# Optimization experiments

Measured on AMD Instinct MI355X. Metric: run time of the kernel, lower is better.

## Reference

```python
import jax, jax.numpy as jnp
import numpy as np

N_HEAD = 16
N_EMBD = 1024
TIME_EMBD = 64
EPS = 1e-5

def _ln(x, w, b):
    mu = jnp.mean(x, axis=-1, keepdims=True)
    var = jnp.mean(jnp.square(x - mu), axis=-1, keepdims=True)
    return (x - mu) * jax.lax.rsqrt(var + EPS) * w + b

def _gelu(x):
    return jax.nn.gelu(x, approximate=False)

def setup_inputs() -> dict:
    key = jax.random.key(0)
    ks = jax.random.split(key, 12)
    B, T, D, TE = 2, 2048, N_EMBD, TIME_EMBD
    C = D + TE  # 1088
    s = lambda fan_in: 1.0 / np.sqrt(fan_in)
    return {
        "z": jax.random.normal(ks[0], (B, T, D), jnp.float32),
        "t": jax.random.uniform(ks[1], (B,), jnp.float32),
        # time_mlp: Linear(1, TE) -> GELU -> Linear(TE, TE)
        "w_t1": jax.random.normal(ks[2], (1, TE), jnp.float32) * s(1),
        "b_t1": jnp.zeros((TE,), jnp.float32),
        "w_t2": jax.random.normal(ks[3], (TE, TE), jnp.float32) * s(TE),
        "b_t2": jnp.zeros((TE,), jnp.float32),
        # attention
        "ln_a_w": jnp.ones((C,), jnp.float32),
        "ln_a_b": jnp.zeros((C,), jnp.float32),
        "w_attn": jax.random.normal(ks[4], (C, 3 * D), jnp.float32) * s(C),
        "b_attn": jnp.zeros((3 * D,), jnp.float32),
        "w_proj": jax.random.normal(ks[5], (D, D), jnp.float32) * s(D),
        "b_proj": jnp.zeros((D,), jnp.float32),
        # mlp
        "ln_m_w": jnp.ones((C,), jnp.float32),
        "ln_m_b": jnp.zeros((C,), jnp.float32),
        "w_fc": jax.random.normal(ks[6], (C, 4 * D), jnp.float32) * s(C),
        "b_fc": jnp.zeros((4 * D,), jnp.float32),
        "w_fc2": jax.random.normal(ks[7], (4 * D, D), jnp.float32) * s(4 * D),
        "b_fc2": jnp.zeros((D,), jnp.float32),
    }

def reference(z, t, w_t1, b_t1, w_t2, b_t2, ln_a_w, ln_a_b, w_attn, b_attn,
              w_proj, b_proj, ln_m_w, ln_m_b, w_fc, b_fc, w_fc2, b_fc2):
    B, T, D = z.shape
    H, hd = N_HEAD, N_EMBD // N_HEAD
    # time embedding: [B, TE] broadcast over T
    t_emb = _gelu(t[:, None] @ w_t1 + b_t1) @ w_t2 + b_t2
    t_emb_bt = jnp.broadcast_to(t_emb[:, None, :], (B, T, TIME_EMBD))
    # --- attention with time-conditioned input ---
    zt = jnp.concatenate([z, t_emb_bt], axis=-1)            # [B,T,D+TE]
    x = _ln(zt, ln_a_w, ln_a_b)
    qkv = x @ w_attn + b_attn                               # [B,T,3D]
    q, k, v = jnp.split(qkv, 3, axis=-1)
    q = q.reshape(B, T, H, hd)
    k = k.reshape(B, T, H, hd)
    v = v.reshape(B, T, H, hd)
    att = jnp.einsum('bqhd,bkhd->bhqk', q, k) * (1.0 / np.sqrt(hd))
    mask = jnp.tril(jnp.ones((T, T), bool))
    att = jnp.where(mask, att, -jnp.inf)
    att = jax.nn.softmax(att, axis=-1)
    y = jnp.einsum('bhqk,bkhd->bqhd', att, v).reshape(B, T, D)
    h = y @ w_proj + b_proj                                 # [B,T,D]
    # --- mlp with time-conditioned input ---
    ht = jnp.concatenate([h, t_emb_bt], axis=-1)
    m = _ln(ht, ln_m_w, ln_m_b)
    dz = _gelu(m @ w_fc + b_fc) @ w_fc2 + b_fc2             # [B,T,D]
    return dz
```

## Files before the change

kernel.cpp:

```cpp
#include <hip/hip_runtime.h>
#include <stdint.h>
#include <math.h>

#define T_SEQ 2048
#define NHEAD 16
#define HD 64
#define DMODEL 1024
#define CDIM 1088
#define MROWS 4096

typedef uint16_t u16;
typedef __bf16 b8v __attribute__((ext_vector_type(8)));
typedef float f4v __attribute__((ext_vector_type(4)));

typedef __attribute__((address_space(3))) void lds_void;
typedef const __attribute__((address_space(1))) void glb_void;

__device__ __forceinline__ float b2f(u16 u) {
  union { uint32_t i; float f; } c; c.i = ((uint32_t)u) << 16; return c.f;
}
__device__ __forceinline__ u16 f2b(float f) {
  union { float f; uint32_t i; } c; c.f = f;
  uint32_t x = c.i;
  return (u16)((x + 0x7fffu + ((x >> 16) & 1u)) >> 16);
}
__device__ __forceinline__ float gelu_f(float x) {
  return 0.5f * x * (1.0f + erff(x * 0.70710678118654752f));
}

__global__ void time_mlp_kernel(const float* __restrict__ t, const float* __restrict__ w1,
                                const float* __restrict__ b1, const float* __restrict__ w2,
                                const float* __restrict__ b2, float* __restrict__ temb) {
  __shared__ float h1[2][64];
  int tid = threadIdx.x;
  int b = tid >> 6, i = tid & 63;
  float tv = t[b];
  h1[b][i] = gelu_f(tv * w1[i] + b1[i]);
  __syncthreads();
  float acc = b2[i];
  for (int k = 0; k < 64; ++k) acc += h1[b][k] * w2[k * 64 + i];
  temb[b * 64 + i] = acc;
}

__global__ __launch_bounds__(256) void transpose_kernel(const float* __restrict__ src,
                                                        u16* __restrict__ dst,
                                                        int R, int C) {
  __shared__ u16 tile[32][33];
  int tx = threadIdx.x & 31, ty = threadIdx.x >> 5;
  int c0 = blockIdx.x * 32, r0 = blockIdx.y * 32;
#pragma unroll
  for (int i = 0; i < 4; ++i) {
    int r = ty + i * 8;
    tile[r][tx] = f2b(src[(size_t)(r0 + r) * C + c0 + tx]);
  }
  __syncthreads();
#pragma unroll
  for (int i = 0; i < 4; ++i) {
    int c = ty + i * 8;
    dst[(size_t)(c0 + c) * R + r0 + tx] = tile[tx][c];
  }
}

__global__ __launch_bounds__(256) void ln_concat_kernel(const float* __restrict__ zf,
                                                        const u16* __restrict__ zb,
                                                        const float* __restrict__ temb,
                                                        const float* __restrict__ w,
                                                        const float* __restrict__ bvec,
                                                        u16* __restrict__ xout,
                                                        int in_f32) {
  __shared__ float red[4];
  int row = blockIdx.x;
  int b = row / T_SEQ;
  int tid = threadIdx.x;
  float v[5];
  float sum = 0.f;
#pragma unroll
  for (int i = 0; i < 5; ++i) {
    int c = tid + i * 256;
    float val = 0.f;
    if (c < CDIM) {
      if (c < DMODEL)
        val = in_f32 ? zf[(size_t)row * DMODEL + c] : b2f(zb[(size_t)row * DMODEL + c]);
      else
        val = temb[b * 64 + (c - DMODEL)];
    }
    v[i] = val;
    sum += val;
  }
#pragma unroll
  for (int off = 32; off; off >>= 1) sum += __shfl_xor(sum, off, 64);
  int wv = tid >> 6, ln = tid & 63;
  if (ln == 0) red[wv] = sum;
  __syncthreads();
  float mean = (red[0] + red[1] + red[2] + red[3]) * (1.0f / CDIM);
  __syncthreads();
  float sq = 0.f;
#pragma unroll
  for (int i = 0; i < 5; ++i) {
    int c = tid + i * 256;
    if (c < CDIM) { float d = v[i] - mean; sq += d * d; }
  }
#pragma unroll
  for (int off = 32; off; off >>= 1) sq += __shfl_xor(sq, off, 64);
  if (ln == 0) red[wv] = sq;
  __syncthreads();
  float inv = rsqrtf((red[0] + red[1] + red[2] + red[3]) * (1.0f / CDIM) + 1e-5f);
#pragma unroll
  for (int i = 0; i < 5; ++i) {
    int c = tid + i * 256;
    if (c < CDIM)
      xout[(size_t)row * CDIM + c] = f2b((v[i] - mean) * inv * w[c] + bvec[c]);
  }
}

__global__ __launch_bounds__(256) void gemm_bt_kernel(const u16* __restrict__ A,
                                                      const u16* __restrict__ Bt,
                                                      const float* __restrict__ bias,
                                                      void* __restrict__ Cout,
                                                      int M, int N, int K,
                                                      int do_gelu, int out_f32) {
  __shared__ u16 As[2][128 * 32];
  __shared__ u16 Bs[2][128 * 32];
  const int tid = threadIdx.x;
  const int wave = tid >> 6, lane = tid & 63;
  const int wr = wave >> 1, wc = wave & 1;
  const int m0 = blockIdx.x * 128;
  const int n0 = blockIdx.y * 128;
  const int lrow = lane & 15, quad = lane >> 4;
  const int srow = lane >> 2, sseg = lane & 3;

  const u16* gA0 = A  + (size_t)(m0 + wave * 32 + srow) * K + sseg * 8;
  const u16* gA1 = gA0 + (size_t)16 * K;
  const u16* gB0 = Bt + (size_t)(n0 + wave * 32 + srow) * K + sseg * 8;
  const u16* gB1 = gB0 + (size_t)16 * K;
  const int la0 = (wave * 32) * 32, la1 = (wave * 32 + 16) * 32;

  f4v acc[4][4] = {};

  __builtin_amdgcn_global_load_lds((glb_void*)gA0, (lds_void*)&As[0][la0], 16, 0, 0);
  __builtin_amdgcn_global_load_lds((glb_void*)gA1, (lds_void*)&As[0][la1], 16, 0, 0);
  __builtin_amdgcn_global_load_lds((glb_void*)gB0, (lds_void*)&Bs[0][la0], 16, 0, 0);
  __builtin_amdgcn_global_load_lds((glb_void*)gB1, (lds_void*)&Bs[0][la1], 16, 0, 0);

  int cur = 0;
  for (int k0 = 0; k0 < K; k0 += 32) {
    __syncthreads();
    if (k0 + 32 < K) {
      int nxt = cur ^ 1;
      __builtin_amdgcn_global_load_lds((glb_void*)(gA0 + k0 + 32), (lds_void*)&As[nxt][la0], 16, 0, 0);
      __builtin_amdgcn_global_load_lds((glb_void*)(gA1 + k0 + 32), (lds_void*)&As[nxt][la1], 16, 0, 0);
      __builtin_amdgcn_global_load_lds((glb_void*)(gB0 + k0 + 32), (lds_void*)&Bs[nxt][la0], 16, 0, 0);
      __builtin_amdgcn_global_load_lds((glb_void*)(gB1 + k0 + 32), (lds_void*)&Bs[nxt][la1], 16, 0, 0);
    }
    b8v af[4], bfr[4];
#pragma unroll
    for (int mi = 0; mi < 4; ++mi)
      af[mi] = *(const b8v*)(&As[cur][(wr * 64 + mi * 16 + lrow) * 32 + quad * 8]);
#pragma unroll
    for (int ni = 0; ni < 4; ++ni)
      bfr[ni] = *(const b8v*)(&Bs[cur][(wc * 64 + ni * 16 + lrow) * 32 + quad * 8]);
#pragma unroll
    for (int mi = 0; mi < 4; ++mi)
#pragma unroll
      for (int ni = 0; ni < 4; ++ni)
        acc[mi][ni] = __builtin_amdgcn_mfma_f32_16x16x32_bf16(af[mi], bfr[ni], acc[mi][ni], 0, 0, 0);
    cur ^= 1;
  }

#pragma unroll
  for (int mi = 0; mi < 4; ++mi) {
#pragma unroll
    for (int ni = 0; ni < 4; ++ni) {
      int gcol = n0 + wc * 64 + ni * 16 + lrow;
      float bv = bias[gcol];
#pragma unroll
      for (int r = 0; r < 4; ++r) {
        int grow = m0 + wr * 64 + mi * 16 + quad * 4 + r;
        float v = acc[mi][ni][r] + bv;
        if (do_gelu) v = gelu_f(v);
        if (out_f32)
          ((float*)Cout)[(size_t)grow * N + gcol] = v;
        else
          ((u16*)Cout)[(size_t)grow * N + gcol] = f2b(v);
      }
    }
  }
}

__global__ __launch_bounds__(256) void attn_mfma_kernel(const u16* __restrict__ qkv,
                                                        u16* __restrict__ y) {
  __shared__ u16 Ks[64 * 72];
  __shared__ u16 Vts[64 * 72];
  __shared__ u16 Ps[128 * 72];
  const int bh = blockIdx.x;
  const int b = bh >> 4, h = bh & 15;
  const int yb = blockIdx.y;
  const int qt = (yb < 8) ? (yb * 2) : (31 - yb * 2);
  const int tid = threadIdx.x, w = tid >> 6, lane = tid & 63;
  const int lrow = lane & 15, quad = lane >> 4;
  const int q0 = qt * 128;

  b8v qf[2][2];
#pragma unroll
  for (int s = 0; s < 2; ++s)
#pragma unroll
    for (int dc = 0; dc < 2; ++dc) {
      int row = q0 + w * 32 + s * 16 + lrow;
      qf[s][dc] = *(const b8v*)(qkv + (size_t)(b * T_SEQ + row) * 3072 + h * 64 + dc * 32 + quad * 8);
    }

  f4v oacc[2][4] = {};
  float mst[2][4], lst[2][4];
#pragma unroll
  for (int s = 0; s < 2; ++s)
#pragma unroll
    for (int r = 0; r < 4; ++r) { mst[s][r] = -__builtin_inff(); lst[s][r] = 0.f; }

  const int nch = 2 * qt + 2;
  for (int ct = 0; ct < nch; ++ct) {
    __syncthreads();
    {
      int r = tid >> 2, sg = tid & 3;
      const u16* src = qkv + (size_t)(b * T_SEQ + ct * 64 + r) * 3072 + h * 64 + 1024 + sg * 16;
      uint4 k1 = *(const uint4*)(src);
      uint4 k2 = *(const uint4*)(src + 8);
      *(uint4*)(&Ks[r * 72 + sg * 16]) = k1;
      *(uint4*)(&Ks[r * 72 + sg * 16 + 8]) = k2;
    }
    {
      int pr = tid >> 3, dsg = tid & 7;
      const u16* v0 = qkv + (size_t)(b * T_SEQ + ct * 64 + 2 * pr) * 3072 + h * 64 + 2048 + dsg * 8;
      uint4 a = *(const uint4*)(v0);
      uint4 bb = *(const uint4*)(v0 + 3072);
      uint32_t aw[4] = {a.x, a.y, a.z, a.w};
      uint32_t bw[4] = {bb.x, bb.y, bb.z, bb.w};
#pragma unroll
      for (int j = 0; j < 8; ++j) {
        int d = dsg * 8 + j;
        u16 ae = (u16)(aw[j >> 1] >> ((j & 1) * 16));
        u16 be = (u16)(bw[j >> 1] >> ((j & 1) * 16));
        int keyp = (2 * pr) ^ (((d >> 3) & 7) * 8);
        *(uint32_t*)(&Vts[d * 72 + keyp]) = (uint32_t)ae | ((uint32_t)be << 16);
      }
    }
    __syncthreads();

    f4v sacc[2][4] = {};
    b8v kf[4][2];
#pragma unroll
    for (int ks = 0; ks < 4; ++ks)
#pragma unroll
      for (int dc = 0; dc < 2; ++dc)
        kf[ks][dc] = *(const b8v*)(&Ks[(ks * 16 + lrow) * 72 + dc * 32 + quad * 8]);
#pragma unroll
    for (int s = 0; s < 2; ++s)
#pragma unroll
      for (int ks = 0; ks < 4; ++ks)
#pragma unroll
        for (int dc = 0; dc < 2; ++dc)
          sacc[s][ks] = __builtin_amdgcn_mfma_f32_16x16x32_bf16(qf[s][dc], kf[ks][dc], sacc[s][ks], 0, 0, 0);

    bool diag = (ct >= 2 * qt);
#pragma unroll
    for (int s = 0; s < 2; ++s)
#pragma unroll
      for (int ks = 0; ks < 4; ++ks) {
        int col = ct * 64 + ks * 16 + lrow;
#pragma unroll
        for (int r = 0; r < 4; ++r) {
          float v = sacc[s][ks][r] * 0.125f;
          int row = q0 + w * 32 + s * 16 + quad * 4 + r;
          if (diag && col > row) v = -__builtin_inff();
          sacc[s][ks][r] = v;
        }
      }

#pragma unroll
    for (int s = 0; s < 2; ++s) {
#pragma unroll
      for (int r = 0; r < 4; ++r) {
        float rmax = fmaxf(fmaxf(sacc[s][0][r], sacc[s][1][r]), fmaxf(sacc[s][2][r], sacc[s][3][r]));
#pragma unroll
        for (int off = 1; off < 16; off <<= 1) rmax = fmaxf(rmax, __shfl_xor(rmax, off, 64));
        float mn = fmaxf(mst[s][r], rmax);
        float al = __expf(mst[s][r] - mn);
        mst[s][r] = mn;
        float psum = 0.f;
#pragma unroll
        for (int ks = 0; ks < 4; ++ks) {
          float p = __expf(sacc[s][ks][r] - mn);
          sacc[s][ks][r] = p;
          psum += p;
        }
#pragma unroll
        for (int off = 1; off < 16; off <<= 1) psum += __shfl_xor(psum, off, 64);
        lst[s][r] = lst[s][r] * al + psum;
#pragma unroll
        for (int ds = 0; ds < 4; ++ds) oacc[s][ds][r] *= al;
      }
    }

#pragma unroll
    for (int s = 0; s < 2; ++s)
#pragma unroll
      for (int ks = 0; ks < 4; ++ks)
#pragma unroll
        for (int r = 0; r < 4; ++r)
          Ps[(w * 32 + s * 16 + quad * 4 + r) * 72 + ks * 16 + lrow] = f2b(sacc[s][ks][r]);

    b8v pf[2][2], vf[4][2];
#pragma unroll
    for (int s = 0; s < 2; ++s)
#pragma unroll
      for (int kc = 0; kc < 2; ++kc)
        pf[s][kc] = *(const b8v*)(&Ps[(w * 32 + s * 16 + lrow) * 72 + kc * 32 + quad * 8]);
#pragma unroll
    for (int ds = 0; ds < 4; ++ds)
#pragma unroll
      for (int kc = 0; kc < 2; ++kc) {
        int d = ds * 16 + lrow;
        int off = (kc * 32 + quad * 8) ^ (((d >> 3) & 7) * 8);
        vf[ds][kc] = *(const b8v*)(&Vts[d * 72 + off]);
      }
#pragma unroll
    for (int s = 0; s < 2; ++s)
#pragma unroll
      for (int ds = 0; ds < 4; ++ds)
#pragma unroll
        for (int kc = 0; kc < 2; ++kc)
          oacc[s][ds] = __builtin_amdgcn_mfma_f32_16x16x32_bf16(pf[s][kc], vf[ds][kc], oacc[s][ds], 0, 0, 0);
  }

#pragma unroll
  for (int s = 0; s < 2; ++s)
#pragma unroll
    for (int ds = 0; ds < 4; ++ds)
#pragma unroll
      for (int r = 0; r < 4; ++r) {
        int row = q0 + w * 32 + s * 16 + quad * 4 + r;
        y[(size_t)(b * T_SEQ + row) * DMODEL + h * 64 + ds * 16 + lrow] =
            f2b(oacc[s][ds][r] / lst[s][r]);
      }
}

extern "C" void kernel_launch(void* const* d_in, const int* in_sizes, int n_in,
                              void* d_out, int out_size, void* d_ws, size_t ws_size,
                              hipStream_t stream) {
  const float* z      = (const float*)d_in[0];
  const float* t      = (const float*)d_in[1];
  const float* w_t1   = (const float*)d_in[2];
  const float* b_t1   = (const float*)d_in[3];
  const float* w_t2   = (const float*)d_in[4];
  const float* b_t2   = (const float*)d_in[5];
  const float* ln_a_w = (const float*)d_in[6];
  const float* ln_a_b = (const float*)d_in[7];
  const float* w_attn = (const float*)d_in[8];
  const float* b_attn = (const float*)d_in[9];
  const float* w_proj = (const float*)d_in[10];
  const float* b_proj = (const float*)d_in[11];
  const float* ln_m_w = (const float*)d_in[12];
  const float* ln_m_b = (const float*)d_in[13];
  const float* w_fc   = (const float*)d_in[14];
  const float* b_fc   = (const float*)d_in[15];
  const float* w_fc2  = (const float*)d_in[16];
  const float* b_fc2  = (const float*)d_in[17];

  char* ws = (char*)d_ws;
  float* temb  = (float*)ws;
  u16* wT_attn = (u16*)(ws + 1024);
  u16* wT_proj = wT_attn + (size_t)3072 * 1088;
  u16* wT_fc   = wT_proj + (size_t)1024 * 1024;
  u16* wT_fc2  = wT_fc   + (size_t)4096 * 1088;
  u16* xbuf    = wT_fc2  + (size_t)1024 * 4096;
  u16* big     = xbuf    + (size_t)4096 * 1088;
  u16* ybuf    = big     + (size_t)4096 * 4096;
  u16* hbuf    = ybuf    + (size_t)4096 * 1024;

  time_mlp_kernel<<<dim3(1), dim3(128), 0, stream>>>(t, w_t1, b_t1, w_t2, b_t2, temb);

  transpose_kernel<<<dim3(3072 / 32, 1088 / 32), dim3(256), 0, stream>>>(w_attn, wT_attn, 1088, 3072);
  transpose_kernel<<<dim3(1024 / 32, 1024 / 32), dim3(256), 0, stream>>>(w_proj, wT_proj, 1024, 1024);
  transpose_kernel<<<dim3(4096 / 32, 1088 / 32), dim3(256), 0, stream>>>(w_fc, wT_fc, 1088, 4096);
  transpose_kernel<<<dim3(1024 / 32, 4096 / 32), dim3(256), 0, stream>>>(w_fc2, wT_fc2, 4096, 1024);

  ln_concat_kernel<<<dim3(MROWS), dim3(256), 0, stream>>>(z, (const u16*)nullptr, temb,
                                                          ln_a_w, ln_a_b, xbuf, 1);

  gemm_bt_kernel<<<dim3(MROWS / 128, 3072 / 128), dim3(256), 0, stream>>>(
      xbuf, wT_attn, b_attn, big, MROWS, 3072, 1088, 0, 0);

  attn_mfma_kernel<<<dim3(32, 16), dim3(256), 0, stream>>>(big, ybuf);

  gemm_bt_kernel<<<dim3(MROWS / 128, 1024 / 128), dim3(256), 0, stream>>>(
      ybuf, wT_proj, b_proj, hbuf, MROWS, 1024, 1024, 0, 0);

  ln_concat_kernel<<<dim3(MROWS), dim3(256), 0, stream>>>((const float*)nullptr, hbuf, temb,
                                                          ln_m_w, ln_m_b, xbuf, 0);

  gemm_bt_kernel<<<dim3(MROWS / 128, 4096 / 128), dim3(256), 0, stream>>>(
      xbuf, wT_fc, b_fc, big, MROWS, 4096, 1088, 1, 0);

  gemm_bt_kernel<<<dim3(MROWS / 128, 1024 / 128), dim3(256), 0, stream>>>(
      big, wT_fc2, b_fc2, d_out, MROWS, 1024, 4096, 0, 1);
}
```

Before: 462.3 us.

## Use 64-row query tiles with transposed MFMA operands in attention

The attention kernel now processes 64 query rows per block instead of 128, launching twice as many blocks, scheduled longest-first. Each wave holds one 16-row query slice. Operands to the MFMA are swapped so each lane owns one query column, which turns the row max and sum reductions into two cross-quad shuffles and allows vectorized P and output stores. The goal is better load balance and occupancy plus cheaper softmax reductions. The cost is that K/V tiles are loaded from global memory twice as often overall.

Result: faster. 426.8 us (-7.7%).

```diff
diff --git a/kernel.cpp b/kernel.cpp
--- a/kernel.cpp
+++ b/kernel.cpp
@@ -191,41 +191,31 @@
                                                         u16* __restrict__ y) {
   __shared__ u16 Ks[64 * 72];
   __shared__ u16 Vts[64 * 72];
-  __shared__ u16 Ps[128 * 72];
+  __shared__ u16 Ps[64 * 72];
   const int bh = blockIdx.x;
   const int b = bh >> 4, h = bh & 15;
-  const int yb = blockIdx.y;
-  const int qt = (yb < 8) ? (yb * 2) : (31 - yb * 2);
+  const int qt = 31 - blockIdx.y;
   const int tid = threadIdx.x, w = tid >> 6, lane = tid & 63;
   const int lrow = lane & 15, quad = lane >> 4;
-  const int q0 = qt * 128;
-
-  b8v qf[2][2];
-#pragma unroll
-  for (int s = 0; s < 2; ++s)
-#pragma unroll
-    for (int dc = 0; dc < 2; ++dc) {
-      int row = q0 + w * 32 + s * 16 + lrow;
-      qf[s][dc] = *(const b8v*)(qkv + (size_t)(b * T_SEQ + row) * 3072 + h * 64 + dc * 32 + quad * 8);
-    }
-
-  f4v oacc[2][4] = {};
-  float mst[2][4], lst[2][4];
-#pragma unroll
-  for (int s = 0; s < 2; ++s)
-#pragma unroll
-    for (int r = 0; r < 4; ++r) { mst[s][r] = -__builtin_inff(); lst[s][r] = 0.f; }
-
-  const int nch = 2 * qt + 2;
+  const int q0 = qt * 64;
+  const int qg = q0 + w * 16 + lrow;
+
+  b8v qf[2];
+#pragma unroll
+  for (int dc = 0; dc < 2; ++dc)
+    qf[dc] = *(const b8v*)(qkv + (size_t)(b * T_SEQ + qg) * 3072 + h * 64 + dc * 32 + quad * 8);
+
+  f4v oacc[4] = {};
+  float mrun = -__builtin_inff(), lrun = 0.f;
+
+  const int nch = qt + 1;
   for (int ct = 0; ct < nch; ++ct) {
     __syncthreads();
     {
       int r = tid >> 2, sg = tid & 3;
       const u16* src = qkv + (size_t)(b * T_SEQ + ct * 64 + r) * 3072 + h * 64 + 1024 + sg * 16;
-      uint4 k1 = *(const uint4*)(src);
-      uint4 k2 = *(const uint4*)(src + 8);
-      *(uint4*)(&Ks[r * 72 + sg * 16]) = k1;
-      *(uint4*)(&Ks[r * 72 + sg * 16 + 8]) = k2;
+      *(uint4*)(&Ks[r * 72 + sg * 16]) = *(const uint4*)(src);
+      *(uint4*)(&Ks[r * 72 + sg * 16 + 8]) = *(const uint4*)(src + 8);
     }
     {
       int pr = tid >> 3, dsg = tid & 7;
@@ -245,102 +235,85 @@
     }
     __syncthreads();
 
-    f4v sacc[2][4] = {};
-    b8v kf[4][2];
+    f4v sacc[4] = {};
 #pragma unroll
     for (int ks = 0; ks < 4; ++ks)
 #pragma unroll
-      for (int dc = 0; dc < 2; ++dc)
-        kf[ks][dc] = *(const b8v*)(&Ks[(ks * 16 + lrow) * 72 + dc * 32 + quad * 8]);
-#pragma unroll
-    for (int s = 0; s < 2; ++s)
-#pragma unroll
-      for (int ks = 0; ks < 4; ++ks)
-#pragma unroll
-        for (int dc = 0; dc < 2; ++dc)
-          sacc[s][ks] = __builtin_amdgcn_mfma_f32_16x16x32_bf16(qf[s][dc], kf[ks][dc], sacc[s][ks], 0, 0, 0);
-
-    bool diag = (ct >= 2 * qt);
-#pragma unroll
-    for (int s = 0; s < 2; ++s)
-#pragma unroll
-      for (int ks = 0; ks < 4; ++ks) {
-        int col = ct * 64 + ks * 16 + lrow;
-#pragma unroll
-        for (int r = 0; r < 4; ++r) {
-          float v = sacc[s][ks][r] * 0.125f;
-          int row = q0 + w * 32 + s * 16 + quad * 4 + r;
-          if (diag && col > row) v = -__builtin_inff();
-          sacc[s][ks][r] = v;
-        }
-      }
-
-#pragma unroll
-    for (int s = 0; s < 2; ++s) {
+      for (int dc = 0; dc < 2; ++dc) {
+        b8v kf = *(const b8v*)(&Ks[(ks * 16 + lrow) * 72 + dc * 32 + quad * 8]);
+        sacc[ks] = __builtin_amdgcn_mfma_f32_16x16x32_bf16(kf, qf[dc], sacc[ks], 0, 0, 0);
+      }
+
+    bool diag = (ct == qt);
+#pragma unroll
+    for (int ks = 0; ks < 4; ++ks)
 #pragma unroll
       for (int r = 0; r < 4; ++r) {
-        float rmax = fmaxf(fmaxf(sacc[s][0][r], sacc[s][1][r]), fmaxf(sacc[s][2][r], sacc[s][3][r]));
-#pragma unroll
-        for (int off = 1; off < 16; off <<= 1) rmax = fmaxf(rmax, __shfl_xor(rmax, off, 64));
-        float mn = fmaxf(mst[s][r], rmax);
-        float al = __expf(mst[s][r] - mn);
-        mst[s][r] = mn;
-        float psum = 0.f;
-#pragma unroll
-        for (int ks = 0; ks < 4; ++ks) {
-          float p = __expf(sacc[s][ks][r] - mn);
-          sacc[s][ks][r] = p;
-          psum += p;
-        }
-#pragma unroll
-        for (int off = 1; off < 16; off <<= 1) psum += __shfl_xor(psum, off, 64);
-        lst[s][r] = lst[s][r] * al + psum;
-#pragma unroll
-        for (int ds = 0; ds < 4; ++ds) oacc[s][ds][r] *= al;
-      }
-    }
-
-#pragma unroll
-    for (int s = 0; s < 2; ++s)
-#pragma unroll
-      for (int ks = 0; ks < 4; ++ks)
-#pragma unroll
-        for (int r = 0; r < 4; ++r)
-          Ps[(w * 32 + s * 16 + quad * 4 + r) * 72 + ks * 16 + lrow] = f2b(sacc[s][ks][r]);
-
-    b8v pf[2][2], vf[4][2];
-#pragma unroll
-    for (int s = 0; s < 2; ++s)
-#pragma unroll
-      for (int kc = 0; kc < 2; ++kc)
-        pf[s][kc] = *(const b8v*)(&Ps[(w * 32 + s * 16 + lrow) * 72 + kc * 32 + quad * 8]);
+        float v = sacc[ks][r] * 0.125f;
+        int key = ct * 64 + ks * 16 + quad * 4 + r;
+        if (diag && key > qg) v = -__builtin_inff();
+        sacc[ks][r] = v;
+      }
+
+    float rmax = sacc[0][0];
+#pragma unroll
+    for (int ks = 0; ks < 4; ++ks)
+#pragma unroll
+      for (int r = 0; r < 4; ++r) rmax = fmaxf(rmax, sacc[ks][r]);
+    rmax = fmaxf(rmax, __shfl_xor(rmax, 16, 64));
+    rmax = fmaxf(rmax, __shfl_xor(rmax, 32, 64));
+    float mn = fmaxf(mrun, rmax);
+    float al = __expf(mrun - mn);
+    mrun = mn;
+    float psum = 0.f;
+#pragma unroll
+    for (int ks = 0; ks < 4; ++ks)
+#pragma unroll
+      for (int r = 0; r < 4; ++r) {
+        float p = __expf(sacc[ks][r] - mn);
+        sacc[ks][r] = p;
+        psum += p;
+      }
+    psum += __shfl_xor(psum, 16, 64);
+    psum += __shfl_xor(psum, 32, 64);
+    lrun = lrun * al + psum;
+#pragma unroll
+    for (int ds = 0; ds < 4; ++ds) oacc[ds] *= al;
+
+#pragma unroll
+    for (int ks = 0; ks < 4; ++ks) {
+      ushort4 pw;
+      pw.x = f2b(sacc[ks][0]); pw.y = f2b(sacc[ks][1]);
+      pw.z = f2b(sacc[ks][2]); pw.w = f2b(sacc[ks][3]);
+      *(ushort4*)(&Ps[(w * 16 + lrow) * 72 + ks * 16 + quad * 4]) = pw;
+    }
+
+    b8v pf[2];
+#pragma unroll
+    for (int kc = 0; kc < 2; ++kc)
+      pf[kc] = *(const b8v*)(&Ps[(w * 16 + lrow) * 72 + kc * 32 + quad * 8]);
 #pragma unroll
     for (int ds = 0; ds < 4; ++ds)
 #pragma unroll
       for (int kc = 0; kc < 2; ++kc) {
         int d = ds * 16 + lrow;
         int off = (kc * 32 + quad * 8) ^ (((d >> 3) & 7) * 8);
-        vf[ds][kc] = *(const b8v*)(&Vts[d * 72 + off]);
-      }
-#pragma unroll
-    for (int s = 0; s < 2; ++s)
-#pragma unroll
-      for (int ds = 0; ds < 4; ++ds)
-#pragma unroll
-        for (int kc = 0; kc < 2; ++kc)
-          oacc[s][ds] = __builtin_amdgcn_mfma_f32_16x16x32_bf16(pf[s][kc], vf[ds][kc], oacc[s][ds], 0, 0, 0);
-  }
-
-#pragma unroll
-  for (int s = 0; s < 2; ++s)
-#pragma unroll
-    for (int ds = 0; ds < 4; ++ds)
-#pragma unroll
-      for (int r = 0; r < 4; ++r) {
-        int row = q0 + w * 32 + s * 16 + quad * 4 + r;
-        y[(size_t)(b * T_SEQ + row) * DMODEL + h * 64 + ds * 16 + lrow] =
-            f2b(oacc[s][ds][r] / lst[s][r]);
-      }
+        b8v vfv = *(const b8v*)(&Vts[d * 72 + off]);
+        oacc[ds] = __builtin_amdgcn_mfma_f32_16x16x32_bf16(vfv, pf[kc], oacc[ds], 0, 0, 0);
+      }
+  }
+
+  float rinv = 1.0f / lrun;
+  u16* yrow = y + (size_t)(b * T_SEQ + qg) * DMODEL + h * 64;
+#pragma unroll
+  for (int ds = 0; ds < 4; ++ds) {
+    ushort4 ov;
+    ov.x = f2b(oacc[ds][0] * rinv);
+    ov.y = f2b(oacc[ds][1] * rinv);
+    ov.z = f2b(oacc[ds][2] * rinv);
+    ov.w = f2b(oacc[ds][3] * rinv);
+    *(ushort4*)(yrow + ds * 16 + quad * 4) = ov;
+  }
 }
 
 extern "C" void kernel_launch(void* const* d_in, const int* in_sizes, int n_in,
@@ -389,7 +362,7 @@
   gemm_bt_kernel<<<dim3(MROWS / 128, 3072 / 128), dim3(256), 0, stream>>>(
       xbuf, wT_attn, b_attn, big, MROWS, 3072, 1088, 0, 0);
 
-  attn_mfma_kernel<<<dim3(32, 16), dim3(256), 0, stream>>>(big, ybuf);
+  attn_mfma_kernel<<<dim3(32, 32), dim3(256), 0, stream>>>(big, ybuf);
 
   gemm_bt_kernel<<<dim3(MROWS / 128, 1024 / 128), dim3(256), 0, stream>>>(
       ybuf, wT_proj, b_proj, hbuf, MROWS, 1024, 1024, 0, 0);
```
